# Kernel tuning notes

Measured on AMD Instinct MI355X. Metric: run time of the kernel, lower is better.

The kernel has to match this reference:

```python
import jax, jax.numpy as jnp
import numpy as np

B, S, E = 2, 2048, 2048
H = 16              # num value heads
D = E // H // 2     # = 64, half head dim (Q/K head dim)
LAMBDA_INIT = 0.8 - 0.6 * float(np.exp(-0.3 * 12))
NORM_EPS = 1e-5


def setup_inputs() -> dict:
    key = jax.random.key(0)
    ks = jax.random.split(key, 10)
    std = 0.02
    x = jax.random.normal(ks[0], (B, S, E), jnp.float32)
    Wq = jax.random.normal(ks[1], (E, E), jnp.float32) * std
    Wk = jax.random.normal(ks[2], (E, E), jnp.float32) * std
    Wv = jax.random.normal(ks[3], (E, E), jnp.float32) * std
    Wo = jax.random.normal(ks[4], (E, E), jnp.float32) * std
    lambda_q1 = jax.random.normal(ks[5], (D,), jnp.float32) * 0.1
    lambda_q2 = jax.random.normal(ks[6], (D,), jnp.float32) * 0.1
    lambda_k1 = jax.random.normal(ks[7], (D,), jnp.float32) * 0.1
    lambda_k2 = jax.random.normal(ks[8], (D,), jnp.float32) * 0.1
    norm_w = jnp.ones((2 * D,), jnp.float32)
    # standard RoPE angle table: (S, D//2)
    inv_freq = 1.0 / (10000.0 ** (np.arange(0, D, 2, dtype=np.float32) / D))
    ang = np.outer(np.arange(S, dtype=np.float32), inv_freq)
    freqs_cos = jnp.asarray(np.cos(ang), jnp.float32)
    freqs_sin = jnp.asarray(np.sin(ang), jnp.float32)
    return {"x": x, "Wq": Wq, "Wk": Wk, "Wv": Wv, "Wo": Wo,
            "lambda_q1": lambda_q1, "lambda_q2": lambda_q2,
            "lambda_k1": lambda_k1, "lambda_k2": lambda_k2,
            "norm_w": norm_w, "freqs_cos": freqs_cos, "freqs_sin": freqs_sin,
            "start_pos": 0}


def _rope(t, cos, sin):
    # t: (B, S, nh, D); complex rotation over pairs along last dim
    tr = t.reshape(*t.shape[:-1], -1, 2)
    tre, tim = tr[..., 0], tr[..., 1]
    c = cos[None, :, None, :]
    s = sin[None, :, None, :]
    out_re = tre * c - tim * s
    out_im = tre * s + tim * c
    return jnp.stack([out_re, out_im], axis=-1).reshape(t.shape)


def reference(x, Wq, Wk, Wv, Wo, lambda_q1, lambda_q2, lambda_k1, lambda_k2,
              norm_w, freqs_cos, freqs_sin, start_pos):
    bsz, tgt_len, _ = x.shape
    scaling = D ** (-0.5)
    q = (x @ Wq.T).reshape(bsz, tgt_len, 2 * H, D)
    k = (x @ Wk.T).reshape(bsz, tgt_len, 2 * H, D)
    v = (x @ Wv.T).reshape(bsz, tgt_len, H, 2 * D)
    q = _rope(q, freqs_cos, freqs_sin)
    k = _rope(k, freqs_cos, freqs_sin)
    q = (q * scaling).transpose(0, 2, 1, 3)      # (B, 2H, S, D)
    keys = k.transpose(0, 2, 1, 3)               # (B, 2H, S, D)
    values = v.transpose(0, 2, 1, 3)             # (B, H, S, 2D)
    scores = jnp.einsum('bhsd,bhtd->bhst', q, keys)
    causal = jnp.where(jnp.arange(tgt_len)[None, :] > jnp.arange(tgt_len)[:, None],
                       jnp.float32(-jnp.inf), jnp.float32(0.0))
    scores = scores + causal
    attn = jax.nn.softmax(scores.astype(jnp.float32), axis=-1)
    lam1 = jnp.exp(jnp.sum(lambda_q1 * lambda_k1))
    lam2 = jnp.exp(jnp.sum(lambda_q2 * lambda_k2))
    lambda_full = lam1 - lam2 + LAMBDA_INIT
    attn = attn.reshape(bsz, H, 2, tgt_len, tgt_len)
    attn_diff = attn[:, :, 0] - lambda_full * attn[:, :, 1]   # (B, H, S, S)
    ctx = jnp.einsum('bhst,bhtd->bhsd', attn_diff, values)    # (B, H, S, 2D)
    # per-head RMSNorm over 2D channel dim
    ctx = ctx * jax.lax.rsqrt(jnp.mean(ctx * ctx, axis=-1, keepdims=True) + NORM_EPS)
    ctx = ctx * norm_w
    ctx = ctx.transpose(0, 2, 1, 3).reshape(bsz, tgt_len, H * 2 * D)
    return ctx @ Wo.T
```

## Files before the change

kernel.cpp:

```cpp
#include <hip/hip_runtime.h>
#include <hip/hip_bf16.h>
#include <stdint.h>

typedef __hip_bfloat16 bf16;
typedef __attribute__((ext_vector_type(8))) short short8;
typedef __attribute__((ext_vector_type(4))) short s4v;
typedef __attribute__((ext_vector_type(4))) float floatx4;

#define MFMA16(a, b, c) __builtin_amdgcn_mfma_f32_16x16x32_bf16((a), (b), (c), 0, 0, 0)
#define LAMBDA_INIT_F 0.7836057665f

__device__ __forceinline__ void async16(const void* g, void* l) {
    __builtin_amdgcn_global_load_lds(
        (const __attribute__((address_space(1))) void*)g,
        (__attribute__((address_space(3))) void*)(uintptr_t)l,
        16, 0, 0);
}

__device__ __forceinline__ float loadf(const void* p, size_t idx, int isbf) {
    if (isbf) return __bfloat162float(((const bf16*)p)[idx]);
    return ((const float*)p)[idx];
}

__global__ void detect_dtype(const unsigned short* __restrict__ x, int* __restrict__ flag) {
    const int t = threadIdx.x;
    const unsigned short u = x[2 * t];
    const int e = (u >> 7) & 0xFF;
    int sane = (e >= 110 && e <= 130) ? 1 : 0;
#pragma unroll
    for (int m = 32; m > 0; m >>= 1) sane += __shfl_xor(sane, m);
    if (t == 0) flag[0] = (sane >= 32) ? 1 : 0;
}

__global__ __launch_bounds__(256) void to_bf16(const void* __restrict__ src,
                                               bf16* __restrict__ dst, int n,
                                               const int* __restrict__ flag,
                                               int skip_if_bf16) {
    if (skip_if_bf16 && flag[0]) return;
    const int i = (blockIdx.x * 256 + threadIdx.x) * 8;
    if (i >= n) return;
    if (flag[0]) {
        *(short8*)(dst + i) = *(const short8*)((const bf16*)src + i);
    } else {
        const float* f = (const float*)src + i;
        short8 r;
#pragma unroll
        for (int j = 0; j < 8; ++j) {
            bf16 h = __float2bfloat16(f[j]);
            r[j] = __builtin_bit_cast(short, h);
        }
        *(short8*)(dst + i) = r;
    }
}

__device__ __forceinline__ void gemm256_core(const bf16* __restrict__ A,
                                             const bf16* __restrict__ B,
                                             void* __restrict__ C,
                                             int N, int bm, int bnl,
                                             const int* __restrict__ flag,
                                             const void* __restrict__ fcos,
                                             const void* __restrict__ fsin,
                                             int mode, char* lds) {
    const int K = 2048;
    const int NT = K / 32;

    const int tid  = threadIdx.x;
    const int lane = tid & 63;
    const int quad = lane >> 4;
    const int l16  = lane & 15;
    const int w    = tid >> 6;
    const int wr   = w >> 2;
    const int wc   = w & 3;

    const int c0 = tid, c1 = tid + 512;
    const int r0 = c0 >> 2, r1 = c1 >> 2;
    const int kc0 = (c0 & 3) ^ (((r0 >> 3) & 1) << 1);
    const int kc1 = (c1 & 3) ^ (((r1 >> 3) & 1) << 1);
    const bf16* Asrc0 = A + (size_t)(bm * 256 + r0) * K + kc0 * 8;
    const bf16* Asrc1 = A + (size_t)(bm * 256 + r1) * K + kc1 * 8;
    const bf16* Bsrc0 = B + (size_t)(bnl * 256 + r0) * K + kc0 * 8;
    const bf16* Bsrc1 = B + (size_t)(bnl * 256 + r1) * K + kc1 * 8;
    const int dA0 = c0 * 16, dA1 = c1 * 16;
    const int dB0 = 16384 + c0 * 16, dB1 = 16384 + c1 * 16;

    const int swz = (quad * 16) ^ ((l16 & 8) << 2);
    int offA[8], offB[4];
#pragma unroll
    for (int f = 0; f < 8; ++f) offA[f] = (wr * 128 + f * 16 + l16) * 64 + swz;
#pragma unroll
    for (int g = 0; g < 4; ++g) offB[g] = 16384 + (wc * 64 + g * 16 + l16) * 64 + swz;

    floatx4 acc[8][4];
#pragma unroll
    for (int f = 0; f < 8; ++f)
#pragma unroll
        for (int g = 0; g < 4; ++g)
#pragma unroll
            for (int r = 0; r < 4; ++r) acc[f][g][r] = 0.0f;

#pragma unroll
    for (int ts = 0; ts < 2; ++ts) {
        char* slot = lds + ts * 32768;
        async16(Asrc0 + ts * 32, slot + dA0);
        async16(Asrc1 + ts * 32, slot + dA1);
        async16(Bsrc0 + ts * 32, slot + dB0);
        async16(Bsrc1 + ts * 32, slot + dB1);
    }
    asm volatile("s_waitcnt vmcnt(4)" ::: "memory");
    __builtin_amdgcn_s_barrier();
    asm volatile("" ::: "memory");

#pragma unroll 4
    for (int t = 0; t < NT; ++t) {
        char* slot  = lds + (t & 3) * 32768;
        const int ts = t + 2;
        char* wslot = lds + (ts & 3) * 32768;

        short8 af[4], bfv[4];
#pragma unroll
        for (int f = 0; f < 4; ++f) af[f] = *(const short8*)(slot + offA[f]);
#pragma unroll
        for (int g = 0; g < 4; ++g) bfv[g] = *(const short8*)(slot + offB[g]);
        if (ts < NT) {
            async16(Asrc0 + (size_t)ts * 32, wslot + dA0);
            async16(Asrc1 + (size_t)ts * 32, wslot + dA1);
        }
        asm volatile("" ::: "memory");
        __builtin_amdgcn_s_barrier();
        asm volatile("" ::: "memory");
        __builtin_amdgcn_s_setprio(1);
#pragma unroll
        for (int f = 0; f < 4; ++f)
#pragma unroll
            for (int g = 0; g < 4; ++g)
                acc[f][g] = MFMA16(af[f], bfv[g], acc[f][g]);
        __builtin_amdgcn_s_setprio(0);

        short8 af2[4];
#pragma unroll
        for (int f = 0; f < 4; ++f) af2[f] = *(const short8*)(slot + offA[4 + f]);
        if (ts < NT) {
            async16(Bsrc0 + (size_t)ts * 32, wslot + dB0);
            async16(Bsrc1 + (size_t)ts * 32, wslot + dB1);
            asm volatile("s_waitcnt vmcnt(4)" ::: "memory");
        } else {
            asm volatile("s_waitcnt vmcnt(0)" ::: "memory");
        }
        __builtin_amdgcn_s_barrier();
        asm volatile("" ::: "memory");
        __builtin_amdgcn_s_setprio(1);
#pragma unroll
        for (int f = 0; f < 4; ++f)
#pragma unroll
            for (int g = 0; g < 4; ++g)
                acc[4 + f][g] = MFMA16(af2[f], bfv[g], acc[4 + f][g]);
        __builtin_amdgcn_s_setprio(0);
    }

    const int isbf  = flag[0];
    const int mbase = bm * 256 + wr * 128;
    const int nbase = bnl * 256 + wc * 64;
    if (mode == 3) {
#pragma unroll
        for (int f = 0; f < 8; ++f)
#pragma unroll
            for (int g = 0; g < 4; ++g) {
                const int n  = nbase + g * 16 + l16;
                const int m0 = mbase + f * 16 + quad * 4;
                const int bb = m0 >> 11;
                const int s0 = m0 & 2047;
                s4v pk;
#pragma unroll
                for (int r = 0; r < 4; ++r) {
                    bf16 hv = __float2bfloat16(acc[f][g][r]);
                    pk[r] = __builtin_bit_cast(short, hv);
                }
                *(s4v*)((bf16*)C + ((size_t)(bb * 2048 + n)) * 2048 + s0) = pk;
            }
    } else if (mode == 1 || mode == 2) {
        const float qs = (mode == 1) ? 0.125f : 1.0f;
#pragma unroll
        for (int f = 0; f < 8; ++f)
#pragma unroll
            for (int g = 0; g < 4; ++g) {
                const int n   = nbase + g * 16 + l16;
                const int jp  = (n & 63) >> 1;
                const float sg = (n & 1) ? 1.0f : -1.0f;
#pragma unroll
                for (int r = 0; r < 4; ++r) {
                    const int m = mbase + f * 16 + quad * 4 + r;
                    const int s = m & 2047;
                    const float v  = acc[f][g][r];
                    const float pv = __shfl_xor(v, 1);
                    const float ct = loadf(fcos, (size_t)s * 32 + jp, isbf);
                    const float st = loadf(fsin, (size_t)s * 32 + jp, isbf);
                    const float out = (v * ct + sg * pv * st) * qs;
                    ((bf16*)C)[(size_t)m * N + n] = __float2bfloat16(out);
                }
            }
    } else {
        const int c_bf = (mode == 4) ? isbf : 1;
#pragma unroll
        for (int f = 0; f < 8; ++f)
#pragma unroll
            for (int g = 0; g < 4; ++g) {
                const int n = nbase + g * 16 + l16;
#pragma unroll
                for (int r = 0; r < 4; ++r) {
                    const int m = mbase + f * 16 + quad * 4 + r;
                    if (c_bf) ((bf16*)C)[(size_t)m * N + n] = __float2bfloat16(acc[f][g][r]);
                    else      ((float*)C)[(size_t)m * N + n] = acc[f][g][r];
                }
            }
    }
}

__global__ __launch_bounds__(512, 2) void gemm256_qkv(const bf16* __restrict__ A,
                                                      const bf16* __restrict__ Wq_s,
                                                      const bf16* __restrict__ Wk_s,
                                                      const bf16* __restrict__ Wv_s,
                                                      const void* __restrict__ WqR,
                                                      const void* __restrict__ WkR,
                                                      const void* __restrict__ WvR,
                                                      bf16* __restrict__ qbuf,
                                                      bf16* __restrict__ kbuf,
                                                      bf16* __restrict__ vtbuf,
                                                      const int* __restrict__ flag,
                                                      const void* __restrict__ fcos,
                                                      const void* __restrict__ fsin) {
    extern __shared__ char lds[];
    const int wsel = blockIdx.x >> 3;
    const int bnl  = blockIdx.x & 7;
    const int isbf = flag[0];
    const bf16* Bp;
    void* Cp;
    int mode;
    if (wsel == 0)      { Bp = isbf ? (const bf16*)WqR : Wq_s; Cp = qbuf;  mode = 1; }
    else if (wsel == 1) { Bp = isbf ? (const bf16*)WkR : Wk_s; Cp = kbuf;  mode = 2; }
    else                { Bp = isbf ? (const bf16*)WvR : Wv_s; Cp = vtbuf; mode = 3; }
    gemm256_core(A, Bp, Cp, 2048, blockIdx.y, bnl, flag, fcos, fsin, mode, lds);
}

__global__ __launch_bounds__(512, 2) void gemm256_ep(const bf16* __restrict__ A,
                                                     const bf16* __restrict__ B,
                                                     void* __restrict__ C,
                                                     int N,
                                                     const int* __restrict__ flag,
                                                     int mode) {
    extern __shared__ char lds[];
    gemm256_core(A, B, C, N, blockIdx.y, blockIdx.x, flag, nullptr, nullptr, mode, lds);
}

__global__ void lambda_kernel(const void* lq1, const void* lq2,
                              const void* lk1, const void* lk2,
                              float* out, const int* __restrict__ flag) {
    const int isbf = flag[0];
    const int t = threadIdx.x;
    float p1 = loadf(lq1, t, isbf) * loadf(lk1, t, isbf);
    float p2 = loadf(lq2, t, isbf) * loadf(lk2, t, isbf);
#pragma unroll
    for (int m = 32; m > 0; m >>= 1) {
        p1 += __shfl_xor(p1, m);
        p2 += __shfl_xor(p2, m);
    }
    if (t == 0) out[0] = expf(p1) - expf(p2) + LAMBDA_INIT_F;
}

__global__ __launch_bounds__(256) void diff_attn(const bf16* __restrict__ Q,
                                                 const bf16* __restrict__ K,
                                                 const bf16* __restrict__ Vt,
                                                 bf16* __restrict__ ctx,
                                                 const float* __restrict__ lam,
                                                 const void* __restrict__ norm_w,
                                                 const int* __restrict__ flag) {
    __shared__ __align__(16) char smem[55296];
    bf16* K1s = (bf16*)smem;
    bf16* K2s = (bf16*)(smem + 8192);
    bf16* Vs  = (bf16*)(smem + 16384);
    char* pool = smem + 32768;

    const int isbf = flag[0];
    const int tid  = threadIdx.x;
    const int lane = tid & 63;
    const int quad = lane >> 4;
    const int l16  = lane & 15;
    const int w    = tid >> 6;
    const int t7   = l16 & 7;

    const int bidx = blockIdx.x;
    const int c8   = bidx & 7;
    const int r6   = bidx >> 3;
    const int p    = r6 & 15;
    const int grp  = (r6 >> 4) * 8 + c8;
    const int h    = grp & 15;
    const int b    = grp >> 4;

    const float lambda_full = lam[0];
    float nw[8];
#pragma unroll
    for (int j = 0; j < 8; ++j) nw[j] = loadf(norm_w, j * 16 + l16, isbf);

    bf16* P1s = (bf16*)(pool + w * 2816);
    bf16* P2s = (bf16*)(pool + 11264 + w * 2816);

    for (int tsel = 0; tsel < 2; ++tsel) {
        const int qt = tsel ? (31 - p) : p;
        const int q0 = qt * 64;

        __syncthreads();

#pragma unroll
        for (int i = 0; i < 2; ++i) {
            const int c = i * 256 + tid;
            const int row = c >> 3, cc = c & 7;
            const int inner = cc ^ (row & 7);
            async16(Q + ((size_t)(b * 2048 + q0 + row) * 32 + 2 * h) * 64 + inner * 8,
                    pool + c * 16);
            async16(Q + ((size_t)(b * 2048 + q0 + row) * 32 + 2 * h + 1) * 64 + inner * 8,
                    pool + 8192 + c * 16);
        }
        __syncthreads();

        short8 qf1[2], qf2[2];
        {
            const int rho = w * 16 + l16;
#pragma unroll
            for (int c = 0; c < 2; ++c) {
                const int ch = (c * 4 + quad) ^ t7;
                qf1[c] = *(const short8*)(pool + rho * 128 + ch * 16);
                qf2[c] = *(const short8*)(pool + 8192 + rho * 128 + ch * 16);
            }
        }

        floatx4 O1[8], O2[8];
#pragma unroll
        for (int j = 0; j < 8; ++j)
#pragma unroll
            for (int r = 0; r < 4; ++r) { O1[j][r] = 0.0f; O2[j][r] = 0.0f; }
        float lp1[4] = {0.f, 0.f, 0.f, 0.f};
        float lp2[4] = {0.f, 0.f, 0.f, 0.f};

        for (int kt0 = 0; kt0 <= q0; kt0 += 64) {
            __syncthreads();
#pragma unroll
            for (int i = 0; i < 2; ++i) {
                const int c = i * 256 + tid;
                const int row = c >> 3, cc = c & 7;
                const int inner = cc ^ (row & 7);
                async16(K + ((size_t)(b * 2048 + kt0 + row) * 32 + 2 * h) * 64 + inner * 8,
                        (char*)K1s + c * 16);
                async16(K + ((size_t)(b * 2048 + kt0 + row) * 32 + 2 * h + 1) * 64 + inner * 8,
                        (char*)K2s + c * 16);
            }
#pragma unroll
            for (int i = 0; i < 4; ++i) {
                const int c = i * 256 + tid;
                const int d = c >> 3, cc = c & 7;
                const int inner = cc ^ (d & 7);
                async16(Vt + ((size_t)(b * 16 + h) * 128 + d) * 2048 + kt0 + inner * 8,
                        (char*)Vs + c * 16);
            }
            __syncthreads();

            floatx4 s1[4], s2[4];
#pragma unroll
            for (int j = 0; j < 4; ++j)
#pragma unroll
                for (int r = 0; r < 4; ++r) { s1[j][r] = 0.0f; s2[j][r] = 0.0f; }
#pragma unroll
            for (int c = 0; c < 2; ++c) {
                const int ch = ((c * 4 + quad) ^ t7) * 16;
#pragma unroll
                for (int j = 0; j < 4; ++j) {
                    short8 k1f = *(const short8*)((const char*)K1s + (j * 16 + l16) * 128 + ch);
                    s1[j] = MFMA16(qf1[c], k1f, s1[j]);
                    short8 k2f = *(const short8*)((const char*)K2s + (j * 16 + l16) * 128 + ch);
                    s2[j] = MFMA16(qf2[c], k2f, s2[j]);
                }
            }

            if (kt0 == q0) {
#pragma unroll
                for (int j = 0; j < 4; ++j)
#pragma unroll
                    for (int r = 0; r < 4; ++r)
                        if (j * 16 + l16 > w * 16 + quad * 4 + r) {
                            s1[j][r] = -1e30f;
                            s2[j][r] = -1e30f;
                        }
            }

#pragma unroll
            for (int j = 0; j < 4; ++j)
#pragma unroll
                for (int r = 0; r < 4; ++r) {
                    const float e1 = __expf(s1[j][r]);
                    const float e2 = __expf(s2[j][r]);
                    lp1[r] += e1;
                    lp2[r] += e2;
                    P1s[(quad * 4 + r) * 88 + j * 16 + l16] = __float2bfloat16(e1);
                    P2s[(quad * 4 + r) * 88 + j * 16 + l16] = __float2bfloat16(e2);
                }

#pragma unroll
            for (int c = 0; c < 2; ++c) {
                short8 a1 = *(const short8*)((const char*)P1s + l16 * 176 + c * 64 + quad * 16);
                short8 a2 = *(const short8*)((const char*)P2s + l16 * 176 + c * 64 + quad * 16);
                const int ch = ((c * 4 + quad) ^ t7) * 16;
#pragma unroll
                for (int j = 0; j < 8; ++j) {
                    short8 vb = *(const short8*)((const char*)Vs + (j * 16 + l16) * 128 + ch);
                    O1[j] = MFMA16(a1, vb, O1[j]);
                    O2[j] = MFMA16(a2, vb, O2[j]);
                }
            }
        }

#pragma unroll
        for (int r = 0; r < 4; ++r) {
            float t1 = lp1[r], t2 = lp2[r];
            t1 += __shfl_xor(t1, 1); t2 += __shfl_xor(t2, 1);
            t1 += __shfl_xor(t1, 2); t2 += __shfl_xor(t2, 2);
            t1 += __shfl_xor(t1, 4); t2 += __shfl_xor(t2, 4);
            t1 += __shfl_xor(t1, 8); t2 += __shfl_xor(t2, 8);
            const float i1 = 1.0f / t1;
            const float i2 = lambda_full / t2;
            float cv[8];
            float ss = 0.0f;
#pragma unroll
            for (int j = 0; j < 8; ++j) {
                const float v = O1[j][r] * i1 - O2[j][r] * i2;
                cv[j] = v;
                ss += v * v;
            }
            ss += __shfl_xor(ss, 1);
            ss += __shfl_xor(ss, 2);
            ss += __shfl_xor(ss, 4);
            ss += __shfl_xor(ss, 8);
            const float scale = rsqrtf(ss * (1.0f / 128.0f) + 1e-5f);
            const int row = q0 + w * 16 + quad * 4 + r;
            const size_t base = ((size_t)(b * 2048) + row) * 2048 + h * 128;
#pragma unroll
            for (int j = 0; j < 8; ++j)
                ctx[base + j * 16 + l16] = __float2bfloat16(cv[j] * scale * nw[j]);
        }
    }
}

extern "C" void kernel_launch(void* const* d_in, const int* in_sizes, int n_in,
                              void* d_out, int out_size, void* d_ws, size_t ws_size,
                              hipStream_t stream) {
    const void* x   = d_in[0];
    const void* Wq  = d_in[1];
    const void* Wk  = d_in[2];
    const void* Wv  = d_in[3];
    const void* Wo  = d_in[4];
    const void* lq1 = d_in[5];
    const void* lq2 = d_in[6];
    const void* lk1 = d_in[7];
    const void* lk2 = d_in[8];
    const void* nw  = d_in[9];
    const void* fc  = d_in[10];
    const void* fs  = d_in[11];

    const size_t BUF = (size_t)4096 * 2048 * sizeof(bf16);
    if (ws_size < 4 * BUF + 64) return;
    char* ws = (char*)d_ws;
    bf16*  qbuf  = (bf16*)(ws);
    bf16*  kbuf  = (bf16*)(ws + BUF);
    bf16*  vbuf  = (bf16*)(ws + 2 * BUF);
    bf16*  vtbuf = (bf16*)(ws + 3 * BUF);
    float* lamb  = (float*)(ws + 4 * BUF);
    int*   flag  = (int*)(ws + 4 * BUF + 8);
    bf16*  xb    = vbuf;
    bf16*  ctxb  = vbuf;

    bf16* wq_s = (bf16*)d_out;
    bf16* wk_s = wq_s + (size_t)2048 * 2048;
    bf16* wv_s = wk_s + (size_t)2048 * 2048;

    const int NX = 2 * 2048 * 2048;
    const int NW = 2048 * 2048;

    hipFuncSetAttribute(reinterpret_cast<const void*>(gemm256_qkv),
                        hipFuncAttributeMaxDynamicSharedMemorySize, 131072);
    hipFuncSetAttribute(reinterpret_cast<const void*>(gemm256_ep),
                        hipFuncAttributeMaxDynamicSharedMemorySize, 131072);

    detect_dtype<<<1, 64, 0, stream>>>((const unsigned short*)x, flag);
    to_bf16<<<NX / 2048, 256, 0, stream>>>(x, xb, NX, flag, 0);

    to_bf16<<<NW / 2048, 256, 0, stream>>>(Wq, wq_s, NW, flag, 1);
    to_bf16<<<NW / 2048, 256, 0, stream>>>(Wk, wk_s, NW, flag, 1);
    to_bf16<<<NW / 2048, 256, 0, stream>>>(Wv, wv_s, NW, flag, 1);

    dim3 gq(24, 16);
    gemm256_qkv<<<gq, 512, 131072, stream>>>(xb, wq_s, wk_s, wv_s, Wq, Wk, Wv,
                                             qbuf, kbuf, vtbuf, flag, fc, fs);

    lambda_kernel<<<1, 64, 0, stream>>>(lq1, lq2, lk1, lk2, lamb, flag);

    diff_attn<<<512, 256, 0, stream>>>(qbuf, kbuf, vtbuf, ctxb, lamb, nw, flag);

    to_bf16<<<NW / 2048, 256, 0, stream>>>(Wo, qbuf, NW, flag, 0);
    dim3 gf(8, 16);
    gemm256_ep<<<gf, 512, 131072, stream>>>(ctxb, qbuf, d_out, 2048, flag, 4);
}
```

Measured before the change: 489.5 us.

## Restructure GEMM mainloop to 64-wide K tiles with four-phase interleaved prefetch

The 256x256 bf16 GEMM core moves from 32-wide K tiles in four rotating LDS slots to 64-wide K tiles in two double-buffered 64KB slots. LDS rows use an 8-way XOR swizzle, and A and B are split into 128-row halves. Each tile runs four MFMA sub-phases, each overlapped with fragment reads and async global-to-LDS loads for the next tiles. The aim is fewer barriers and waitcnts per unit of K work and better overlap of memory with MFMA. The cost is more barriers inside each tile, more live fragment registers, and a tight slot-reuse schedule where a synchronisation mistake would give wrong results.

New measurement: 542.4 us. +10.8%, slower.

```diff
diff --git a/kernel.cpp b/kernel.cpp
--- a/kernel.cpp
+++ b/kernel.cpp
@@ -9,6 +9,7 @@
 
 #define MFMA16(a, b, c) __builtin_amdgcn_mfma_f32_16x16x32_bf16((a), (b), (c), 0, 0, 0)
 #define LAMBDA_INIT_F 0.7836057665f
+#define FENCE() asm volatile("" ::: "memory")
 
 __device__ __forceinline__ void async16(const void* g, void* l) {
     __builtin_amdgcn_global_load_lds(
@@ -61,8 +62,8 @@
                                              const void* __restrict__ fcos,
                                              const void* __restrict__ fsin,
                                              int mode, char* lds) {
-    const int K = 2048;
-    const int NT = K / 32;
+    const int K  = 2048;
+    const int NT = 32;
 
     const int tid  = threadIdx.x;
     const int lane = tid & 63;
@@ -73,22 +74,26 @@
     const int wc   = w & 3;
 
     const int c0 = tid, c1 = tid + 512;
-    const int r0 = c0 >> 2, r1 = c1 >> 2;
-    const int kc0 = (c0 & 3) ^ (((r0 >> 3) & 1) << 1);
-    const int kc1 = (c1 & 3) ^ (((r1 >> 3) & 1) << 1);
-    const bf16* Asrc0 = A + (size_t)(bm * 256 + r0) * K + kc0 * 8;
-    const bf16* Asrc1 = A + (size_t)(bm * 256 + r1) * K + kc1 * 8;
-    const bf16* Bsrc0 = B + (size_t)(bnl * 256 + r0) * K + kc0 * 8;
-    const bf16* Bsrc1 = B + (size_t)(bnl * 256 + r1) * K + kc1 * 8;
-    const int dA0 = c0 * 16, dA1 = c1 * 16;
-    const int dB0 = 16384 + c0 * 16, dB1 = 16384 + c1 * 16;
-
-    const int swz = (quad * 16) ^ ((l16 & 8) << 2);
-    int offA[8], offB[4];
-#pragma unroll
-    for (int f = 0; f < 8; ++f) offA[f] = (wr * 128 + f * 16 + l16) * 64 + swz;
-#pragma unroll
-    for (int g = 0; g < 4; ++g) offB[g] = 16384 + (wc * 64 + g * 16 + l16) * 64 + swz;
+    const int r0 = c0 >> 3, r1 = c1 >> 3;
+    const int ks0 = ((c0 & 7) ^ (r0 & 7)) * 8;
+    const int ks1 = ((c1 & 7) ^ (r1 & 7)) * 8;
+    const bf16* A0s0 = A + (size_t)(bm * 256 + r0) * K + ks0;
+    const bf16* A0s1 = A + (size_t)(bm * 256 + r1) * K + ks1;
+    const bf16* A1s0 = A + (size_t)(bm * 256 + 128 + r0) * K + ks0;
+    const bf16* A1s1 = A + (size_t)(bm * 256 + 128 + r1) * K + ks1;
+    const bf16* B0s0 = B + (size_t)(bnl * 256 + r0) * K + ks0;
+    const bf16* B0s1 = B + (size_t)(bnl * 256 + r1) * K + ks1;
+    const bf16* B1s0 = B + (size_t)(bnl * 256 + 128 + r0) * K + ks0;
+    const bf16* B1s1 = B + (size_t)(bnl * 256 + 128 + r1) * K + ks1;
+    const int dst0 = c0 * 16, dst1 = c1 * 16;
+
+    const int swzc  = l16 & 7;
+    const int colk0 = ((0 + quad) ^ swzc) * 16;
+    const int colk1 = ((4 + quad) ^ swzc) * 16;
+    const int aB[2] = { wr * 16384 + l16 * 128 + colk0,
+                        wr * 16384 + l16 * 128 + colk1 };
+    const int bB[2] = { 32768 + (wc >> 1) * 16384 + ((wc & 1) * 64 + l16) * 128 + colk0,
+                        32768 + (wc >> 1) * 16384 + ((wc & 1) * 64 + l16) * 128 + colk1 };
 
     floatx4 acc[8][4];
 #pragma unroll
@@ -98,64 +103,131 @@
 #pragma unroll
             for (int r = 0; r < 4; ++r) acc[f][g][r] = 0.0f;
 
-#pragma unroll
-    for (int ts = 0; ts < 2; ++ts) {
-        char* slot = lds + ts * 32768;
-        async16(Asrc0 + ts * 32, slot + dA0);
-        async16(Asrc1 + ts * 32, slot + dA1);
-        async16(Bsrc0 + ts * 32, slot + dB0);
-        async16(Bsrc1 + ts * 32, slot + dB1);
-    }
+    char* slot0 = lds;
+    char* slot1 = lds + 65536;
+
+    async16(B0s0, slot0 + 32768 + dst0);  async16(B0s1, slot0 + 32768 + dst1);
+    async16(B1s0, slot0 + 49152 + dst0);  async16(B1s1, slot0 + 49152 + dst1);
+    async16(A0s0, slot0 + 0     + dst0);  async16(A0s1, slot0 + 0     + dst1);
+    async16(A1s0, slot0 + 16384 + dst0);  async16(A1s1, slot0 + 16384 + dst1);
+    async16(B0s0 + 64, slot1 + 32768 + dst0);  async16(B0s1 + 64, slot1 + 32768 + dst1);
+    async16(B1s0 + 64, slot1 + 49152 + dst0);  async16(B1s1 + 64, slot1 + 49152 + dst1);
     asm volatile("s_waitcnt vmcnt(4)" ::: "memory");
     __builtin_amdgcn_s_barrier();
-    asm volatile("" ::: "memory");
-
-#pragma unroll 4
-    for (int t = 0; t < NT; ++t) {
-        char* slot  = lds + (t & 3) * 32768;
-        const int ts = t + 2;
-        char* wslot = lds + (ts & 3) * 32768;
-
-        short8 af[4], bfv[4];
-#pragma unroll
-        for (int f = 0; f < 4; ++f) af[f] = *(const short8*)(slot + offA[f]);
-#pragma unroll
-        for (int g = 0; g < 4; ++g) bfv[g] = *(const short8*)(slot + offB[g]);
-        if (ts < NT) {
-            async16(Asrc0 + (size_t)ts * 32, wslot + dA0);
-            async16(Asrc1 + (size_t)ts * 32, wslot + dA1);
-        }
-        asm volatile("" ::: "memory");
-        __builtin_amdgcn_s_barrier();
-        asm volatile("" ::: "memory");
+    FENCE();
+
+    auto tile_body = [&](int tt, char* cur, char* oth) {
+        const int t1 = (tt + 1 < NT) ? tt + 1 : NT - 1;
+        const int t2 = (tt + 2 < NT) ? tt + 2 : NT - 1;
+        const size_t k1 = (size_t)t1 * 64;
+        const size_t k2 = (size_t)t2 * 64;
+
+        short8 a03[4][2], a47[4][2], bb[4][2];
+
+#pragma unroll
+        for (int f = 0; f < 4; ++f)
+#pragma unroll
+            for (int kh = 0; kh < 2; ++kh)
+                a03[f][kh] = *(const short8*)(cur + aB[kh] + f * 2048);
+#pragma unroll
+        for (int g = 0; g < 2; ++g)
+#pragma unroll
+            for (int kh = 0; kh < 2; ++kh)
+                bb[g][kh] = *(const short8*)(cur + bB[kh] + g * 2048);
+        async16(A0s0 + k1, oth + 0 + dst0);
+        async16(A0s1 + k1, oth + 0 + dst1);
+        FENCE();
+        __builtin_amdgcn_s_barrier();
+        FENCE();
         __builtin_amdgcn_s_setprio(1);
 #pragma unroll
         for (int f = 0; f < 4; ++f)
 #pragma unroll
-            for (int g = 0; g < 4; ++g)
-                acc[f][g] = MFMA16(af[f], bfv[g], acc[f][g]);
+            for (int g = 0; g < 2; ++g) {
+                acc[f][g] = MFMA16(a03[f][0], bb[g][0], acc[f][g]);
+                acc[f][g] = MFMA16(a03[f][1], bb[g][1], acc[f][g]);
+            }
         __builtin_amdgcn_s_setprio(0);
-
-        short8 af2[4];
-#pragma unroll
-        for (int f = 0; f < 4; ++f) af2[f] = *(const short8*)(slot + offA[4 + f]);
-        if (ts < NT) {
-            async16(Bsrc0 + (size_t)ts * 32, wslot + dB0);
-            async16(Bsrc1 + (size_t)ts * 32, wslot + dB1);
-            asm volatile("s_waitcnt vmcnt(4)" ::: "memory");
-        } else {
-            asm volatile("s_waitcnt vmcnt(0)" ::: "memory");
-        }
-        __builtin_amdgcn_s_barrier();
-        asm volatile("" ::: "memory");
+        FENCE();
+        __builtin_amdgcn_s_barrier();
+        FENCE();
+
+#pragma unroll
+        for (int g = 2; g < 4; ++g)
+#pragma unroll
+            for (int kh = 0; kh < 2; ++kh)
+                bb[g][kh] = *(const short8*)(cur + bB[kh] + g * 2048);
+#pragma unroll
+        for (int f = 0; f < 2; ++f)
+#pragma unroll
+            for (int kh = 0; kh < 2; ++kh)
+                a47[f][kh] = *(const short8*)(cur + aB[kh] + (4 + f) * 2048);
+        async16(A1s0 + k1, oth + 16384 + dst0);
+        async16(A1s1 + k1, oth + 16384 + dst1);
+        FENCE();
+        __builtin_amdgcn_s_barrier();
+        FENCE();
         __builtin_amdgcn_s_setprio(1);
 #pragma unroll
         for (int f = 0; f < 4; ++f)
 #pragma unroll
-            for (int g = 0; g < 4; ++g)
-                acc[4 + f][g] = MFMA16(af2[f], bfv[g], acc[4 + f][g]);
+            for (int g = 2; g < 4; ++g) {
+                acc[f][g] = MFMA16(a03[f][0], bb[g][0], acc[f][g]);
+                acc[f][g] = MFMA16(a03[f][1], bb[g][1], acc[f][g]);
+            }
         __builtin_amdgcn_s_setprio(0);
+        FENCE();
+        __builtin_amdgcn_s_barrier();
+        FENCE();
+
+#pragma unroll
+        for (int f = 2; f < 4; ++f)
+#pragma unroll
+            for (int kh = 0; kh < 2; ++kh)
+                a47[f][kh] = *(const short8*)(cur + aB[kh] + (4 + f) * 2048);
+        async16(B0s0 + k2, cur + 32768 + dst0);
+        async16(B0s1 + k2, cur + 32768 + dst1);
+        FENCE();
+        __builtin_amdgcn_s_barrier();
+        FENCE();
+        __builtin_amdgcn_s_setprio(1);
+#pragma unroll
+        for (int f = 0; f < 4; ++f)
+#pragma unroll
+            for (int g = 0; g < 2; ++g) {
+                acc[4 + f][g] = MFMA16(a47[f][0], bb[g][0], acc[4 + f][g]);
+                acc[4 + f][g] = MFMA16(a47[f][1], bb[g][1], acc[4 + f][g]);
+            }
+        __builtin_amdgcn_s_setprio(0);
+        FENCE();
+        __builtin_amdgcn_s_barrier();
+        FENCE();
+
+        async16(B1s0 + k2, cur + 49152 + dst0);
+        async16(B1s1 + k2, cur + 49152 + dst1);
+        asm volatile("s_waitcnt vmcnt(4)" ::: "memory");
+        __builtin_amdgcn_s_barrier();
+        FENCE();
+        __builtin_amdgcn_s_setprio(1);
+#pragma unroll
+        for (int f = 0; f < 4; ++f)
+#pragma unroll
+            for (int g = 2; g < 4; ++g) {
+                acc[4 + f][g] = MFMA16(a47[f][0], bb[g][0], acc[4 + f][g]);
+                acc[4 + f][g] = MFMA16(a47[f][1], bb[g][1], acc[4 + f][g]);
+            }
+        __builtin_amdgcn_s_setprio(0);
+        FENCE();
+        __builtin_amdgcn_s_barrier();
+        FENCE();
+    };
+
+    for (int u = 0; u < NT; u += 2) {
+        tile_body(u,     slot0, slot1);
+        tile_body(u + 1, slot1, slot0);
     }
+    asm volatile("s_waitcnt vmcnt(0)" ::: "memory");
+    FENCE();
 
     const int isbf  = flag[0];
     const int mbase = bm * 256 + wr * 128;
@@ -167,7 +239,7 @@
             for (int g = 0; g < 4; ++g) {
                 const int n  = nbase + g * 16 + l16;
                 const int m0 = mbase + f * 16 + quad * 4;
-                const int bb = m0 >> 11;
+                const int bb2 = m0 >> 11;
                 const int s0 = m0 & 2047;
                 s4v pk;
 #pragma unroll
@@ -175,7 +247,7 @@
                     bf16 hv = __float2bfloat16(acc[f][g][r]);
                     pk[r] = __builtin_bit_cast(short, hv);
                 }
-                *(s4v*)((bf16*)C + ((size_t)(bb * 2048 + n)) * 2048 + s0) = pk;
+                *(s4v*)((bf16*)C + ((size_t)(bb2 * 2048 + n)) * 2048 + s0) = pk;
             }
     } else if (mode == 1 || mode == 2) {
         const float qs = (mode == 1) ? 0.125f : 1.0f;
```

## Use 128-wide N tiles for output GEMM, fuse input conversions, swizzle blocks

Applied to the files above, without the earlier changes.

The output projection GEMM moves to a templated core with 256x128 tiles, doubling the grid from 128 to 256 blocks so more CUs are busy. The separate x/Wq/Wk/Wv conversion launches are merged into one kernel. Block indices in both GEMMs are remapped for better L2 reuse, and the Wo conversion is skipped when inputs are already bf16. Smaller tiles lower arithmetic intensity per block in exchange for better CU fill.

Result: faster. 465.6 us (-4.9%).

```diff
diff --git a/kernel.cpp b/kernel.cpp
--- a/kernel.cpp
+++ b/kernel.cpp
@@ -9,6 +9,7 @@
 
 #define MFMA16(a, b, c) __builtin_amdgcn_mfma_f32_16x16x32_bf16((a), (b), (c), 0, 0, 0)
 #define LAMBDA_INIT_F 0.7836057665f
+#define FENCE() asm volatile("" ::: "memory")
 
 __device__ __forceinline__ void async16(const void* g, void* l) {
     __builtin_amdgcn_global_load_lds(
@@ -30,6 +31,40 @@
 #pragma unroll
     for (int m = 32; m > 0; m >>= 1) sane += __shfl_xor(sane, m);
     if (t == 0) flag[0] = (sane >= 32) ? 1 : 0;
+}
+
+__device__ __forceinline__ void conv_body(const void* src, bf16* dst, int boff,
+                                          int isbf) {
+    const int i = (boff * 256 + threadIdx.x) * 8;
+    if (isbf) {
+        *(short8*)(dst + i) = *(const short8*)((const bf16*)src + i);
+    } else {
+        const float* f = (const float*)src + i;
+        short8 r;
+#pragma unroll
+        for (int j = 0; j < 8; ++j) {
+            bf16 h = __float2bfloat16(f[j]);
+            r[j] = __builtin_bit_cast(short, h);
+        }
+        *(short8*)(dst + i) = r;
+    }
+}
+
+__global__ __launch_bounds__(256) void convert_all(const void* __restrict__ x,
+                                                   const void* __restrict__ Wq,
+                                                   const void* __restrict__ Wk,
+                                                   const void* __restrict__ Wv,
+                                                   bf16* __restrict__ xb,
+                                                   bf16* __restrict__ wq,
+                                                   bf16* __restrict__ wk,
+                                                   bf16* __restrict__ wv,
+                                                   const int* __restrict__ flag) {
+    const int bid  = blockIdx.x;
+    const int isbf = flag[0];
+    if (bid < 4096)      { conv_body(x, xb, bid, isbf); }
+    else if (bid < 6144) { if (isbf) return; conv_body(Wq, wq, bid - 4096, 0); }
+    else if (bid < 8192) { if (isbf) return; conv_body(Wk, wk, bid - 6144, 0); }
+    else                 { if (isbf) return; conv_body(Wv, wv, bid - 8192, 0); }
 }
 
 __global__ __launch_bounds__(256) void to_bf16(const void* __restrict__ src,
@@ -39,21 +74,11 @@
     if (skip_if_bf16 && flag[0]) return;
     const int i = (blockIdx.x * 256 + threadIdx.x) * 8;
     if (i >= n) return;
-    if (flag[0]) {
-        *(short8*)(dst + i) = *(const short8*)((const bf16*)src + i);
-    } else {
-        const float* f = (const float*)src + i;
-        short8 r;
-#pragma unroll
-        for (int j = 0; j < 8; ++j) {
-            bf16 h = __float2bfloat16(f[j]);
-            r[j] = __builtin_bit_cast(short, h);
-        }
-        *(short8*)(dst + i) = r;
-    }
-}
-
-__device__ __forceinline__ void gemm256_core(const bf16* __restrict__ A,
+    conv_body(src, dst, blockIdx.x, flag[0]);
+}
+
+template <int BNT>
+__device__ __forceinline__ void gemm_core256(const bf16* __restrict__ A,
                                              const bf16* __restrict__ B,
                                              void* __restrict__ C,
                                              int N, int bm, int bnl,
@@ -61,16 +86,22 @@
                                              const void* __restrict__ fcos,
                                              const void* __restrict__ fsin,
                                              int mode, char* lds) {
-    const int K = 2048;
-    const int NT = K / 32;
+    constexpr int K    = 2048;
+    constexpr int NT   = 64;
+    constexpr int ASZ  = 16384;
+    constexpr int BSZ  = BNT * 64;
+    constexpr int SLOT = ASZ + BSZ;
+    constexpr int F    = (BNT == 256) ? 8 : 4;
+    constexpr int FH   = F / 2;
+    constexpr int BCH  = BNT / 128;
 
     const int tid  = threadIdx.x;
     const int lane = tid & 63;
     const int quad = lane >> 4;
     const int l16  = lane & 15;
     const int w    = tid >> 6;
-    const int wr   = w >> 2;
-    const int wc   = w & 3;
+    const int wr   = (BNT == 256) ? (w >> 2) : (w >> 1);
+    const int wc   = (BNT == 256) ? (w & 3) : (w & 1);
 
     const int c0 = tid, c1 = tid + 512;
     const int r0 = c0 >> 2, r1 = c1 >> 2;
@@ -78,21 +109,21 @@
     const int kc1 = (c1 & 3) ^ (((r1 >> 3) & 1) << 1);
     const bf16* Asrc0 = A + (size_t)(bm * 256 + r0) * K + kc0 * 8;
     const bf16* Asrc1 = A + (size_t)(bm * 256 + r1) * K + kc1 * 8;
-    const bf16* Bsrc0 = B + (size_t)(bnl * 256 + r0) * K + kc0 * 8;
-    const bf16* Bsrc1 = B + (size_t)(bnl * 256 + r1) * K + kc1 * 8;
+    const bf16* Bsrc0 = B + (size_t)(bnl * BNT + r0) * K + kc0 * 8;
+    const bf16* Bsrc1 = B + (size_t)(bnl * BNT + r1) * K + kc1 * 8;
     const int dA0 = c0 * 16, dA1 = c1 * 16;
-    const int dB0 = 16384 + c0 * 16, dB1 = 16384 + c1 * 16;
+    const int dB0 = ASZ + c0 * 16, dB1 = ASZ + c1 * 16;
 
     const int swz = (quad * 16) ^ ((l16 & 8) << 2);
     int offA[8], offB[4];
 #pragma unroll
-    for (int f = 0; f < 8; ++f) offA[f] = (wr * 128 + f * 16 + l16) * 64 + swz;
-#pragma unroll
-    for (int g = 0; g < 4; ++g) offB[g] = 16384 + (wc * 64 + g * 16 + l16) * 64 + swz;
-
-    floatx4 acc[8][4];
-#pragma unroll
-    for (int f = 0; f < 8; ++f)
+    for (int f = 0; f < F; ++f) offA[f] = (wr * (F * 16) + f * 16 + l16) * 64 + swz;
+#pragma unroll
+    for (int g = 0; g < 4; ++g) offB[g] = ASZ + (wc * 64 + g * 16 + l16) * 64 + swz;
+
+    floatx4 acc[F][4];
+#pragma unroll
+    for (int f = 0; f < F; ++f)
 #pragma unroll
         for (int g = 0; g < 4; ++g)
 #pragma unroll
@@ -100,74 +131,76 @@
 
 #pragma unroll
     for (int ts = 0; ts < 2; ++ts) {
-        char* slot = lds + ts * 32768;
+        char* slot = lds + ts * SLOT;
         async16(Asrc0 + ts * 32, slot + dA0);
         async16(Asrc1 + ts * 32, slot + dA1);
         async16(Bsrc0 + ts * 32, slot + dB0);
-        async16(Bsrc1 + ts * 32, slot + dB1);
+        if constexpr (BCH == 2) async16(Bsrc1 + ts * 32, slot + dB1);
     }
-    asm volatile("s_waitcnt vmcnt(4)" ::: "memory");
+    if constexpr (BNT == 256) asm volatile("s_waitcnt vmcnt(4)" ::: "memory");
+    else                      asm volatile("s_waitcnt vmcnt(3)" ::: "memory");
     __builtin_amdgcn_s_barrier();
-    asm volatile("" ::: "memory");
+    FENCE();
 
 #pragma unroll 4
     for (int t = 0; t < NT; ++t) {
-        char* slot  = lds + (t & 3) * 32768;
+        char* slot  = lds + (t & 3) * SLOT;
         const int ts = t + 2;
-        char* wslot = lds + (ts & 3) * 32768;
-
-        short8 af[4], bfv[4];
-#pragma unroll
-        for (int f = 0; f < 4; ++f) af[f] = *(const short8*)(slot + offA[f]);
+        char* wslot = lds + (ts & 3) * SLOT;
+
+        short8 af[FH], bfv[4];
+#pragma unroll
+        for (int f = 0; f < FH; ++f) af[f] = *(const short8*)(slot + offA[f]);
 #pragma unroll
         for (int g = 0; g < 4; ++g) bfv[g] = *(const short8*)(slot + offB[g]);
         if (ts < NT) {
             async16(Asrc0 + (size_t)ts * 32, wslot + dA0);
             async16(Asrc1 + (size_t)ts * 32, wslot + dA1);
         }
-        asm volatile("" ::: "memory");
+        FENCE();
         __builtin_amdgcn_s_barrier();
-        asm volatile("" ::: "memory");
+        FENCE();
         __builtin_amdgcn_s_setprio(1);
 #pragma unroll
-        for (int f = 0; f < 4; ++f)
+        for (int f = 0; f < FH; ++f)
 #pragma unroll
             for (int g = 0; g < 4; ++g)
                 acc[f][g] = MFMA16(af[f], bfv[g], acc[f][g]);
         __builtin_amdgcn_s_setprio(0);
 
-        short8 af2[4];
-#pragma unroll
-        for (int f = 0; f < 4; ++f) af2[f] = *(const short8*)(slot + offA[4 + f]);
+        short8 af2[FH];
+#pragma unroll
+        for (int f = 0; f < FH; ++f) af2[f] = *(const short8*)(slot + offA[FH + f]);
         if (ts < NT) {
             async16(Bsrc0 + (size_t)ts * 32, wslot + dB0);
-            async16(Bsrc1 + (size_t)ts * 32, wslot + dB1);
-            asm volatile("s_waitcnt vmcnt(4)" ::: "memory");
+            if constexpr (BCH == 2) async16(Bsrc1 + (size_t)ts * 32, wslot + dB1);
+            if constexpr (BNT == 256) asm volatile("s_waitcnt vmcnt(4)" ::: "memory");
+            else                      asm volatile("s_waitcnt vmcnt(3)" ::: "memory");
         } else {
             asm volatile("s_waitcnt vmcnt(0)" ::: "memory");
         }
         __builtin_amdgcn_s_barrier();
-        asm volatile("" ::: "memory");
+        FENCE();
         __builtin_amdgcn_s_setprio(1);
 #pragma unroll
-        for (int f = 0; f < 4; ++f)
+        for (int f = 0; f < FH; ++f)
 #pragma unroll
             for (int g = 0; g < 4; ++g)
-                acc[4 + f][g] = MFMA16(af2[f], bfv[g], acc[4 + f][g]);
+                acc[FH + f][g] = MFMA16(af2[f], bfv[g], acc[FH + f][g]);
         __builtin_amdgcn_s_setprio(0);
     }
 
     const int isbf  = flag[0];
-    const int mbase = bm * 256 + wr * 128;
-    const int nbase = bnl * 256 + wc * 64;
+    const int mbase = bm * 256 + wr * (F * 16);
+    const int nbase = bnl * BNT + wc * 64;
     if (mode == 3) {
 #pragma unroll
-        for (int f = 0; f < 8; ++f)
+        for (int f = 0; f < F; ++f)
 #pragma unroll
             for (int g = 0; g < 4; ++g) {
                 const int n  = nbase + g * 16 + l16;
                 const int m0 = mbase + f * 16 + quad * 4;
-                const int bb = m0 >> 11;
+                const int bb2 = m0 >> 11;
                 const int s0 = m0 & 2047;
                 s4v pk;
 #pragma unroll
@@ -175,12 +208,12 @@
                     bf16 hv = __float2bfloat16(acc[f][g][r]);
                     pk[r] = __builtin_bit_cast(short, hv);
                 }
-                *(s4v*)((bf16*)C + ((size_t)(bb * 2048 + n)) * 2048 + s0) = pk;
+                *(s4v*)((bf16*)C + ((size_t)(bb2 * 2048 + n)) * 2048 + s0) = pk;
             }
     } else if (mode == 1 || mode == 2) {
         const float qs = (mode == 1) ? 0.125f : 1.0f;
 #pragma unroll
-        for (int f = 0; f < 8; ++f)
+        for (int f = 0; f < F; ++f)
 #pragma unroll
             for (int g = 0; g < 4; ++g) {
                 const int n   = nbase + g * 16 + l16;
@@ -201,7 +234,7 @@
     } else {
         const int c_bf = (mode == 4) ? isbf : 1;
 #pragma unroll
-        for (int f = 0; f < 8; ++f)
+        for (int f = 0; f < F; ++f)
 #pragma unroll
             for (int g = 0; g < 4; ++g) {
                 const int n = nbase + g * 16 + l16;
@@ -229,8 +262,12 @@
                                                       const void* __restrict__ fcos,
                                                       const void* __restrict__ fsin) {
     extern __shared__ char lds[];
-    const int wsel = blockIdx.x >> 3;
-    const int bnl  = blockIdx.x & 7;
+    const int flat = blockIdx.y * 24 + blockIdx.x;
+    const int swz  = (flat & 7) * 48 + (flat >> 3);
+    const int wsel = swz >> 7;
+    const int rem  = swz & 127;
+    const int bm   = rem >> 3;
+    const int bnl  = rem & 7;
     const int isbf = flag[0];
     const bf16* Bp;
     void* Cp;
@@ -238,17 +275,21 @@
     if (wsel == 0)      { Bp = isbf ? (const bf16*)WqR : Wq_s; Cp = qbuf;  mode = 1; }
     else if (wsel == 1) { Bp = isbf ? (const bf16*)WkR : Wk_s; Cp = kbuf;  mode = 2; }
     else                { Bp = isbf ? (const bf16*)WvR : Wv_s; Cp = vtbuf; mode = 3; }
-    gemm256_core(A, Bp, Cp, 2048, blockIdx.y, bnl, flag, fcos, fsin, mode, lds);
-}
-
-__global__ __launch_bounds__(512, 2) void gemm256_ep(const bf16* __restrict__ A,
-                                                     const bf16* __restrict__ B,
-                                                     void* __restrict__ C,
-                                                     int N,
-                                                     const int* __restrict__ flag,
-                                                     int mode) {
+    gemm_core256<256>(A, Bp, Cp, 2048, bm, bnl, flag, fcos, fsin, mode, lds);
+}
+
+__global__ __launch_bounds__(512, 2) void gemm128_fin(const bf16* __restrict__ A,
+                                                      const bf16* __restrict__ Wo_s,
+                                                      const void* __restrict__ WoR,
+                                                      void* __restrict__ C,
+                                                      const int* __restrict__ flag) {
     extern __shared__ char lds[];
-    gemm256_core(A, B, C, N, blockIdx.y, blockIdx.x, flag, nullptr, nullptr, mode, lds);
+    const int flat = blockIdx.y * 16 + blockIdx.x;
+    const int swz  = (flat & 7) * 32 + (flat >> 3);
+    const int bm   = swz >> 4;
+    const int bnl  = swz & 15;
+    const bf16* Bp = flag[0] ? (const bf16*)WoR : Wo_s;
+    gemm_core256<128>(A, Bp, C, 2048, bm, bnl, flag, nullptr, nullptr, 4, lds);
 }
 
 __global__ void lambda_kernel(const void* lq1, const void* lq2,
@@ -479,20 +520,15 @@
     bf16* wk_s = wq_s + (size_t)2048 * 2048;
     bf16* wv_s = wk_s + (size_t)2048 * 2048;
 
-    const int NX = 2 * 2048 * 2048;
     const int NW = 2048 * 2048;
 
     hipFuncSetAttribute(reinterpret_cast<const void*>(gemm256_qkv),
                         hipFuncAttributeMaxDynamicSharedMemorySize, 131072);
-    hipFuncSetAttribute(reinterpret_cast<const void*>(gemm256_ep),
-                        hipFuncAttributeMaxDynamicSharedMemorySize, 131072);
+    hipFuncSetAttribute(reinterpret_cast<const void*>(gemm128_fin),
+                        hipFuncAttributeMaxDynamicSharedMemorySize, 98304);
 
     detect_dtype<<<1, 64, 0, stream>>>((const unsigned short*)x, flag);
-    to_bf16<<<NX / 2048, 256, 0, stream>>>(x, xb, NX, flag, 0);
-
-    to_bf16<<<NW / 2048, 256, 0, stream>>>(Wq, wq_s, NW, flag, 1);
-    to_bf16<<<NW / 2048, 256, 0, stream>>>(Wk, wk_s, NW, flag, 1);
-    to_bf16<<<NW / 2048, 256, 0, stream>>>(Wv, wv_s, NW, flag, 1);
+    convert_all<<<10240, 256, 0, stream>>>(x, Wq, Wk, Wv, xb, wq_s, wk_s, wv_s, flag);
 
     dim3 gq(24, 16);
     gemm256_qkv<<<gq, 512, 131072, stream>>>(xb, wq_s, wk_s, wv_s, Wq, Wk, Wv,
@@ -502,7 +538,7 @@
 
     diff_attn<<<512, 256, 0, stream>>>(qbuf, kbuf, vtbuf, ctxb, lamb, nw, flag);
 
-    to_bf16<<<NW / 2048, 256, 0, stream>>>(Wo, qbuf, NW, flag, 0);
-    dim3 gf(8, 16);
-    gemm256_ep<<<gf, 512, 131072, stream>>>(ctxb, qbuf, d_out, 2048, flag, 4);
-}
+    to_bf16<<<NW / 2048, 256, 0, stream>>>(Wo, qbuf, NW, flag, 1);
+    dim3 gf(16, 16);
+    gemm128_fin<<<gf, 512, 98304, stream>>>(ctxb, qbuf, Wo, d_out, flag);
+}
```
